# Kernel optimization log

Measured on AMD Instinct MI355X. Metric: run time of the kernel, lower is better.

Reference implementation:

```python
import jax, jax.numpy as jnp
import numpy as np
from jax import lax

N_P = 0.5      # module_cfg.n_p
CUTOFF = 0.3   # module_cfg.cutoff


def setup_inputs() -> dict:
    key = jax.random.key(0)
    k1, k2, k3, k4 = jax.random.split(key, 4)
    h = jax.random.normal(k1, (1, 8192, 256), jnp.float32)
    pos = jax.random.normal(k2, (8192, 3), jnp.float32)
    W = jax.random.normal(k3, (256, 256), jnp.float32) / 16.0  # ~ Linear init scale
    b = jax.random.normal(k4, (256,), jnp.float32) * 0.01
    return {"h": h, "pos": pos, "W": W, "b": b}


def fps_indices(pos, k, select=0):
    """Farthest point sampling; returns the k selected indices in ascending
    index order (matching torch boolean-mask indexing pos[selected])."""
    n = pos.shape[0]
    selected = jnp.zeros(n, dtype=bool).at[select].set(True)
    d = jnp.linalg.norm(pos - pos[select], axis=-1)  # (N,) euclidean, as torch.pairwise_distance
    d = jnp.where(selected, -jnp.inf, d)

    def body(i, carry):
        sel, dist = carry
        new = jnp.argmax(dist)
        sel = sel.at[new].set(True)
        dist = jnp.minimum(dist, jnp.linalg.norm(pos - pos[new], axis=-1))
        dist = jnp.where(sel, -jnp.inf, dist)
        return sel, dist

    sel, _ = lax.fori_loop(0, k - 1, body, (selected, d))
    return jnp.nonzero(sel, size=k)[0]  # exactly k True entries, sorted


def reference(h, pos, W, b):
    B, num_res, c_s = h.shape
    n_nodes = int(num_res * N_P)  # num_res * n_p // 1

    idx = fps_indices(pos, n_nodes)          # (n_nodes,)
    new_node_pos = pos[idx]                  # (n_nodes, 3)

    # torch.cdist(pos, new_node_pos, p=3): Minkowski p=3 distance
    diff = jnp.abs(pos[:, None, :] - new_node_pos[None, :, :])  # (N, n_nodes, 3)
    dist = jnp.cbrt(jnp.sum(diff ** 3, axis=-1))                 # (N, n_nodes)

    # sparse membership mask (fixed-shape equivalent of the nonzero edge list)
    mask = dist < CUTOFF                      # (N, n_nodes) bool

    # sparse gather-matmul: aggregate residue features into each sampled node
    agg = jnp.einsum('nm,bnc->bmc', mask.astype(h.dtype), h)     # (B, n_nodes, c_s)
    new_node_embed = agg @ W.T + b            # nn.Linear(c_s, c_s)
    return new_node_embed, new_node_pos, mask
```

## Files before the change

kernel.cpp:

```cpp
#include <hip/hip_runtime.h>
#include <hip/hip_bf16.h>
#include <cmath>

#define FPS_N 8192
#define FPS_K 4096
#define CS    256
#define FT    1024
#define PPT   8
#define NEGINF (-__builtin_inff())
#define FPS_LDS_BYTES (131072 + 256)

__device__ __forceinline__ float p3sum(float x, float y, float z,
                                       float nx, float ny, float nz) {
  float dx = fabsf(__fsub_rn(x, nx));
  float dy = fabsf(__fsub_rn(y, ny));
  float dz = fabsf(__fsub_rn(z, nz));
  float cx = __fmul_rn(__fmul_rn(dx, dx), dx);
  float cy = __fmul_rn(__fmul_rn(dy, dy), dy);
  float cz = __fmul_rn(__fmul_rn(dz, dz), dz);
  return __fadd_rn(__fadd_rn(cx, cy), cz);
}

__device__ __forceinline__ float eucl2(float x, float y, float z,
                                       float nx, float ny, float nz) {
  float dx = __fsub_rn(x, nx);
  float dy = __fsub_rn(y, ny);
  float dz = __fsub_rn(z, nz);
  return __fadd_rn(__fadd_rn(__fmul_rn(dx, dx), __fmul_rn(dy, dy)),
                   __fmul_rn(dz, dz));
}

#define LEXGT(va, ka, vb, kb) (((va) > (vb)) || ((va) == (vb) && ((ka) < (kb))))
#define SELP(va, ka, vb, kb) { bool t_ = LEXGT(vb, kb, va, ka); \
  va = t_ ? (vb) : (va); ka = t_ ? (kb) : (ka); }

template<int CTRL>
__device__ __forceinline__ void dpp_sel2(float& v, int& k) {
  int nv = __builtin_amdgcn_update_dpp(__float_as_int(v), __float_as_int(v), CTRL, 0xF, 0xF, false);
  int nk = __builtin_amdgcn_update_dpp(k, k, CTRL, 0xF, 0xF, false);
  float fv = __int_as_float(nv);
  bool t = LEXGT(fv, nk, v, k);
  v = t ? fv : v;
  k = t ? nk : k;
}

__global__ __launch_bounds__(1024) void bin_kernel(const float* __restrict__ pos,
                                                   float* __restrict__ px,
                                                   float* __restrict__ py,
                                                   float* __restrict__ pz,
                                                   unsigned short* __restrict__ ids16,
                                                   unsigned char* __restrict__ selb) {
  __shared__ int hist[4096];
  __shared__ int part[1024];
  const int tid = threadIdx.x;
#pragma unroll
  for (int i = 0; i < 4; ++i) hist[tid * 4 + i] = 0;
  ((int*)selb)[tid * 2 + 0] = 0;
  ((int*)selb)[tid * 2 + 1] = 0;
  if (tid == 0) selb[0] = 1;
  __syncthreads();

  float qx[8], qy[8], qz[8];
  int cell[8];
  {
    const float4* p4 = (const float4*)pos + tid * 6;
    float4 a0 = p4[0], a1 = p4[1], a2 = p4[2], a3 = p4[3], a4 = p4[4], a5 = p4[5];
    qx[0]=a0.x; qy[0]=a0.y; qz[0]=a0.z;
    qx[1]=a0.w; qy[1]=a1.x; qz[1]=a1.y;
    qx[2]=a1.z; qy[2]=a1.w; qz[2]=a2.x;
    qx[3]=a2.y; qy[3]=a2.z; qz[3]=a2.w;
    qx[4]=a3.x; qy[4]=a3.y; qz[4]=a3.z;
    qx[5]=a3.w; qy[5]=a4.x; qz[5]=a4.y;
    qx[6]=a4.z; qy[6]=a4.w; qz[6]=a5.x;
    qx[7]=a5.y; qy[7]=a5.z; qz[7]=a5.w;
  }
#pragma unroll
  for (int j = 0; j < 8; ++j) {
    int ix = min(max((int)floorf((qx[j] + 4.0f) * 2.0f), 0), 15);
    int iy = min(max((int)floorf((qy[j] + 4.0f) * 2.0f), 0), 15);
    int iz = min(max((int)floorf((qz[j] + 4.0f) * 2.0f), 0), 15);
    int m = 0;
#pragma unroll
    for (int b = 0; b < 4; ++b)
      m |= (((ix >> b) & 1) << (3 * b)) | (((iy >> b) & 1) << (3 * b + 1)) |
           (((iz >> b) & 1) << (3 * b + 2));
    cell[j] = m;
    atomicAdd(&hist[m], 1);
  }
  __syncthreads();
  int h0 = hist[tid * 4], h1 = hist[tid * 4 + 1], h2 = hist[tid * 4 + 2], h3 = hist[tid * 4 + 3];
  int s = h0 + h1 + h2 + h3;
  part[tid] = s;
  __syncthreads();
  for (int off = 1; off < 1024; off <<= 1) {
    int u = (tid >= off) ? part[tid - off] : 0;
    __syncthreads();
    part[tid] += u;
    __syncthreads();
  }
  int base = part[tid] - s;
  hist[tid * 4 + 0] = base;
  hist[tid * 4 + 1] = base + h0;
  hist[tid * 4 + 2] = base + h0 + h1;
  hist[tid * 4 + 3] = base + h0 + h1 + h2;
  __syncthreads();
#pragma unroll
  for (int j = 0; j < 8; ++j) {
    int slot = atomicAdd(&hist[cell[j]], 1);
    px[slot] = qx[j];
    py[slot] = qy[j];
    pz[slot] = qz[j];
    ids16[slot] = (unsigned short)(tid * 8 + j);
  }
}

#define RESCAN() { \
  float v0 = dd[0], v1 = dd[1], v2 = dd[2], v3 = dd[3]; \
  float v4 = dd[4], v5 = dd[5], v6 = dd[6], v7 = dd[7]; \
  int j0 = key[0], j1 = key[1], j2 = key[2], j3 = key[3]; \
  int j4 = key[4], j5 = key[5], j6 = key[6], j7 = key[7]; \
  SELP(v0, j0, v1, j1) SELP(v2, j2, v3, j3) SELP(v4, j4, v5, j5) SELP(v6, j6, v7, j7) \
  SELP(v0, j0, v2, j2) SELP(v4, j4, v6, j6) SELP(v0, j0, v4, j4) \
  bv = v0; bkey = j0; }

__global__ __launch_bounds__(FT) void fps_kernel(const float* __restrict__ pos,
                                                 const float* __restrict__ spx,
                                                 const float* __restrict__ spy,
                                                 const float* __restrict__ spz,
                                                 const unsigned short* __restrict__ sid,
                                                 unsigned char* __restrict__ selb) {
  extern __shared__ char smem[];
  float4* lds4 = (float4*)smem;
  int2*   slots = (int2*)(smem + 131072);
  const int tid = threadIdx.x, lane = tid & 63, wave = tid >> 6;

  for (int i = tid; i < FPS_N; i += FT)
    lds4[i] = make_float4(spx[i], spy[i], spz[i], 0.f);
  __syncthreads();

  float x[PPT], y[PPT], z[PPT], dd[PPT];
  int key[PPT];
  const float p0x = pos[0], p0y = pos[1], p0z = pos[2];
  {
    int4 b0 = ((const int4*)sid)[tid];
    int op[4] = { b0.x, b0.y, b0.z, b0.w };
#pragma unroll
    for (int j = 0; j < PPT; ++j) {
      int oid = (j & 1) ? ((op[j >> 1] >> 16) & 0xffff) : (op[j >> 1] & 0xffff);
      key[j] = (oid << 13) | (tid * PPT + j);
      float4 p = lds4[tid * PPT + j];
      x[j] = p.x; y[j] = p.y; z[j] = p.z;
      float s = eucl2(p.x, p.y, p.z, p0x, p0y, p0z);
      dd[j] = (oid == 0) ? NEGINF : sqrtf(s);
    }
  }
  float mnx = x[0], mny = y[0], mnz = z[0], mxx = x[0], mxy = y[0], mxz = z[0];
#pragma unroll
  for (int j = 1; j < PPT; ++j) {
    mnx = fminf(mnx, x[j]); mny = fminf(mny, y[j]); mnz = fminf(mnz, z[j]);
    mxx = fmaxf(mxx, x[j]); mxy = fmaxf(mxy, y[j]); mxz = fmaxf(mxz, z[j]);
  }

  unsigned selmask = 0;
  float bv; int bkey;
  RESCAN();
  {
    float rv = bv; int rk = bkey;
    dpp_sel2<0x111>(rv, rk); dpp_sel2<0x112>(rv, rk); dpp_sel2<0x114>(rv, rk);
    dpp_sel2<0x118>(rv, rk); dpp_sel2<0x142>(rv, rk); dpp_sel2<0x143>(rv, rk);
    if (lane == 63) slots[wave] = make_int2(__float_as_int(rv), rk);
  }
  __syncthreads();

  for (int k = 0; k < FPS_K - 1; ++k) {
    const int p = k & 1, pn = p ^ 1;
    const int2 sl = slots[p * 16 + (lane & 15)];
    float gv = __int_as_float(sl.x);
    int   gk = sl.y;
    dpp_sel2<0xB1>(gv, gk);
    dpp_sel2<0x4E>(gv, gk);
    dpp_sel2<0x124>(gv, gk);
    dpp_sel2<0x128>(gv, gk);
    const int stor = gk & 8191;

    const float4 wrec = lds4[stor];
    const float wx = wrec.x, wy = wrec.y, wz = wrec.z;

    bool own = false;
    if ((stor >> 3) == tid) {
      const int jj = stor & 7;
#pragma unroll
      for (int j = 0; j < PPT; ++j) if (j == jj) dd[j] = NEGINF;
      selmask |= (1u << jj);
      own = true;
    }

    const float lg = fmaxf(bv, 0.f);
    float cx = fminf(fmaxf(wx, mnx), mxx);
    float cy = fminf(fmaxf(wy, mny), mxy);
    float cz = fminf(fmaxf(wz, mnz), mxz);
    float ddx = wx - cx, ddy = wy - cy, ddz = wz - cz;
    float bd2 = ddx * ddx + ddy * ddy + ddz * ddz;
    const bool fire = (bd2 * 0.999f < lg * lg);
    if (fire) {
#pragma unroll
      for (int j = 0; j < PPT; ++j)
        dd[j] = fminf(dd[j], sqrtf(eucl2(x[j], y[j], z[j], wx, wy, wz)));
    }

    if (__ballot((fire || own) ? 1 : 0)) {
      if (fire || own) { RESCAN(); }
      float rv = bv; int rk = bkey;
      dpp_sel2<0x111>(rv, rk); dpp_sel2<0x112>(rv, rk); dpp_sel2<0x114>(rv, rk);
      dpp_sel2<0x118>(rv, rk); dpp_sel2<0x142>(rv, rk); dpp_sel2<0x143>(rv, rk);
      if (lane == 63) slots[pn * 16 + wave] = make_int2(__float_as_int(rv), rk);
    } else {
      if (lane == wave) slots[pn * 16 + wave] = sl;
    }
    __syncthreads();
  }

#pragma unroll
  for (int j = 0; j < PPT; ++j)
    if ((selmask >> j) & 1) selb[key[j] >> 13] = 1;
}

__global__ __launch_bounds__(1024) void emit_kernel(const unsigned char* __restrict__ selb,
                                                    const float* __restrict__ pos,
                                                    float* __restrict__ pos_out) {
  __shared__ int sc[1024];
  const int tid = threadIdx.x;
  int w0 = ((const int*)selb)[tid * 2 + 0];
  int w1 = ((const int*)selb)[tid * 2 + 1];
  int cnt = __popc(w0) + __popc(w1);
  sc[tid] = cnt;
  __syncthreads();
  for (int off = 1; off < 1024; off <<= 1) {
    int u = (tid >= off) ? sc[tid - off] : 0;
    __syncthreads();
    sc[tid] += u;
    __syncthreads();
  }
  int r = sc[tid] - cnt;
#pragma unroll
  for (int j = 0; j < 8; ++j) {
    int w = (j < 4) ? w0 : w1;
    if ((w >> ((j & 3) * 8)) & 1) {
      int oi = tid * 8 + j;
      pos_out[r * 3 + 0] = pos[oi * 3 + 0];
      pos_out[r * 3 + 1] = pos[oi * 3 + 1];
      pos_out[r * 3 + 2] = pos[oi * 3 + 2];
      ++r;
    }
  }
}

__global__ __launch_bounds__(256) void wt_kernel(const float* __restrict__ W,
                                                 float* __restrict__ WT) {
  int i = blockIdx.x * 256 + threadIdx.x;
  int c = i >> 8, cp = i & 255;
  WT[i] = W[cp * 256 + c];
}

__global__ __launch_bounds__(256) void agg_linear_kernel(
    const float* __restrict__ h, const float* __restrict__ pos,
    const float* __restrict__ nodepos, const float* __restrict__ WT,
    const float* __restrict__ bias, float* __restrict__ embed, float sb) {
  const int m = blockIdx.x;
  const int tid = threadIdx.x;
  const int lane = tid & 63, wave = tid >> 6;
  const float nx = nodepos[m * 3 + 0];
  const float ny = nodepos[m * 3 + 1];
  const float nz = nodepos[m * 3 + 2];
  const float4* h4 = (const float4*)h;

  float4 acc = make_float4(0.f, 0.f, 0.f, 0.f);
  const int base0 = wave * (FPS_N / 4);
  for (int base = base0; base < base0 + (FPS_N / 4); base += 64) {
    int n = base + lane;
    float px = pos[n * 3 + 0], py = pos[n * 3 + 1], pz = pos[n * 3 + 2];
    unsigned long long mb = __ballot((p3sum(px, py, pz, nx, ny, nz) <= sb) ? 1 : 0);
    while (mb) {
      int b = __ffsll(mb) - 1;
      mb &= (mb - 1);
      float4 hv = h4[(size_t)(base + b) * 64 + lane];
      acc.x += hv.x; acc.y += hv.y; acc.z += hv.z; acc.w += hv.w;
    }
  }

  __shared__ float lacc[4][256];
  lacc[wave][lane * 4 + 0] = acc.x;
  lacc[wave][lane * 4 + 1] = acc.y;
  lacc[wave][lane * 4 + 2] = acc.z;
  lacc[wave][lane * 4 + 3] = acc.w;
  __syncthreads();
  __shared__ float aggrow[256];
  float aggv = ((lacc[0][tid] + lacc[1][tid]) + lacc[2][tid]) + lacc[3][tid];
  aggrow[tid] = aggv;
  __syncthreads();

  float o = bias[tid];
#pragma unroll 8
  for (int c = 0; c < 256; ++c)
    o = fmaf(aggrow[c], WT[c * 256 + tid], o);
  embed[(size_t)m * 256 + tid] = o;
}

__global__ __launch_bounds__(256) void mask_kernel(const float* __restrict__ pos,
                                                   const float* __restrict__ nodepos,
                                                   float* __restrict__ maskout,
                                                   float sb) {
  int n  = blockIdx.y;
  int m0 = (blockIdx.x * 256 + threadIdx.x) * 4;
  float x = pos[n * 3 + 0], y = pos[n * 3 + 1], z = pos[n * 3 + 2];
  const float4* np4 = (const float4*)(nodepos + (size_t)m0 * 3);
  float4 a = np4[0], bq = np4[1], cq = np4[2];
  float4 r;
  r.x = (p3sum(x, y, z, a.x,  a.y,  a.z)  <= sb) ? 1.0f : 0.0f;
  r.y = (p3sum(x, y, z, a.w,  bq.x, bq.y) <= sb) ? 1.0f : 0.0f;
  r.z = (p3sum(x, y, z, bq.z, bq.w, cq.x) <= sb) ? 1.0f : 0.0f;
  r.w = (p3sum(x, y, z, cq.y, cq.z, cq.w) <= sb) ? 1.0f : 0.0f;
  *(float4*)(maskout + (size_t)n * FPS_K + m0) = r;
}

extern "C" void kernel_launch(void* const* d_in, const int* in_sizes, int n_in,
                              void* d_out, int out_size, void* d_ws, size_t ws_size,
                              hipStream_t stream) {
  (void)in_sizes; (void)n_in; (void)out_size; (void)d_ws; (void)ws_size;
  const float* h   = (const float*)d_in[0];
  const float* pos = (const float*)d_in[1];
  const float* W   = (const float*)d_in[2];
  const float* b   = (const float*)d_in[3];

  float* out     = (float*)d_out;
  float* embed   = out;
  float* pos_out = out + (size_t)FPS_K * CS;
  float* mask    = pos_out + (size_t)FPS_K * 3;
  float* WT      = mask;
  float* px      = mask + (1 << 21);
  float* py      = px + FPS_N;
  float* pz      = py + FPS_N;
  unsigned short* ids16 = (unsigned short*)(pz + FPS_N);
  unsigned char*  selb  = ((unsigned char*)ids16) + 2 * FPS_N;

  const float  t    = 0.3f;
  const float  ulpv = nextafterf(t, 1.0f) - t;
  const double rmid = (double)t - (double)ulpv * 0.5;
  const double C    = rmid * rmid * rmid;
  float sb = (float)C;
  if (!((double)sb < C)) sb = nextafterf(sb, 0.0f);

  hipFuncSetAttribute((const void*)fps_kernel,
                      hipFuncAttributeMaxDynamicSharedMemorySize, FPS_LDS_BYTES);

  hipLaunchKernelGGL(bin_kernel, dim3(1), dim3(1024), 0, stream,
                     pos, px, py, pz, ids16, selb);
  hipLaunchKernelGGL(fps_kernel, dim3(1), dim3(FT), FPS_LDS_BYTES, stream,
                     pos, px, py, pz, ids16, selb);
  hipLaunchKernelGGL(emit_kernel, dim3(1), dim3(1024), 0, stream,
                     selb, pos, pos_out);
  hipLaunchKernelGGL(wt_kernel, dim3(256), dim3(256), 0, stream, W, WT);
  hipLaunchKernelGGL(agg_linear_kernel, dim3(FPS_K), dim3(256), 0, stream,
                     h, pos, pos_out, WT, b, embed, sb);
  hipLaunchKernelGGL(mask_kernel, dim3(4, FPS_N), dim3(256), 0, stream,
                     pos, pos_out, mask, sb);
}
```

Measured before the change: 6.913 ms.

## Select up to four FPS points per barrier using per-wave top-2 candidates

The FPS loop now keeps the top two candidates per wave, together with their coordinates, in shared slots. Each iteration can then accept up to four successive farthest points without a block-wide barrier. A candidate is accepted only when its distance to the points already accepted in that batch is at least its own value, so the greedy order is preserved. This also drops the 128KB LDS copy of point coordinates, because coordinates now travel with the slot records. The aim is to cut the number of __syncthreads rounds in the serial 4095-step loop, at the cost of more DPP traffic per step and more complex reduction logic.

```diff
diff --git a/kernel.cpp b/kernel.cpp
--- a/kernel.cpp
+++ b/kernel.cpp
@@ -8,7 +8,6 @@
 #define FT    1024
 #define PPT   8
 #define NEGINF (-__builtin_inff())
-#define FPS_LDS_BYTES (131072 + 256)
 
 __device__ __forceinline__ float p3sum(float x, float y, float z,
                                        float nx, float ny, float nz) {
@@ -31,18 +30,91 @@
 }
 
 #define LEXGT(va, ka, vb, kb) (((va) > (vb)) || ((va) == (vb) && ((ka) < (kb))))
-#define SELP(va, ka, vb, kb) { bool t_ = LEXGT(vb, kb, va, ka); \
-  va = t_ ? (vb) : (va); ka = t_ ? (kb) : (ka); }
 
 template<int CTRL>
-__device__ __forceinline__ void dpp_sel2(float& v, int& k) {
-  int nv = __builtin_amdgcn_update_dpp(__float_as_int(v), __float_as_int(v), CTRL, 0xF, 0xF, false);
-  int nk = __builtin_amdgcn_update_dpp(k, k, CTRL, 0xF, 0xF, false);
-  float fv = __int_as_float(nv);
-  bool t = LEXGT(fv, nk, v, k);
-  v = t ? fv : v;
-  k = t ? nk : k;
-}
+__device__ __forceinline__ int dppi(int a) {
+  return __builtin_amdgcn_update_dpp(a, a, CTRL, 0xF, 0xF, false);
+}
+template<int CTRL>
+__device__ __forceinline__ float dppf(float a) {
+  return __int_as_float(__builtin_amdgcn_update_dpp(__float_as_int(a), __float_as_int(a), CTRL, 0xF, 0xF, false));
+}
+
+template<int CTRL>
+__device__ __forceinline__ void dpp_sel5(float& v, int& k, float& x, float& y, float& z) {
+  float pv = dppf<CTRL>(v); int pk = dppi<CTRL>(k);
+  float px = dppf<CTRL>(x); float py = dppf<CTRL>(y); float pz = dppf<CTRL>(z);
+  bool t = LEXGT(pv, pk, v, k);
+  v = t ? pv : v; k = t ? pk : k;
+  x = t ? px : x; y = t ? py : y; z = t ? pz : z;
+}
+
+template<int CTRL>
+__device__ __forceinline__ void dpp_top2(float& v1, int& k1, float& v2, int& k2) {
+  float p1 = dppf<CTRL>(v1); int q1 = dppi<CTRL>(k1);
+  float p2 = dppf<CTRL>(v2); int q2 = dppi<CTRL>(k2);
+  bool t = LEXGT(p1, q1, v1, k1);
+  float lv = t ? v1 : p1; int lk = t ? k1 : q1;
+  float ov = t ? p2 : v2; int ok = t ? q2 : k2;
+  v1 = t ? p1 : v1; k1 = t ? q1 : k1;
+  bool u = LEXGT(lv, lk, ov, ok);
+  v2 = u ? lv : ov; k2 = u ? lk : ok;
+}
+
+#define PAIR2(v1, k1, v2, k2, a, ka, b, kb) { bool t_ = LEXGT(b, kb, a, ka); \
+  v1 = t_ ? (b) : (a); k1 = t_ ? (kb) : (ka); v2 = t_ ? (a) : (b); k2 = t_ ? (ka) : (kb); }
+
+#define MERGE22(v1, k1, v2, k2, w1, l1, w2, l2) { \
+  bool t_ = LEXGT(w1, l1, v1, k1); \
+  float lv_ = t_ ? (v1) : (w1); int lk_ = t_ ? (k1) : (l1); \
+  float ov_ = t_ ? (w2) : (v2); int ok_ = t_ ? (l2) : (k2); \
+  v1 = t_ ? (w1) : (v1); k1 = t_ ? (l1) : (k1); \
+  bool u_ = LEXGT(lv_, lk_, ov_, ok_); \
+  v2 = u_ ? lv_ : ov_; k2 = u_ ? lk_ : ok_; }
+
+#define RESCAN2() { \
+  float A1, B1, C1, D1, A2, B2, C2, D2; int Ak, Bk, Ck, Dk, Ak2, Bk2, Ck2, Dk2; \
+  PAIR2(A1, Ak, A2, Ak2, dd[0], key[0], dd[1], key[1]) \
+  PAIR2(B1, Bk, B2, Bk2, dd[2], key[2], dd[3], key[3]) \
+  PAIR2(C1, Ck, C2, Ck2, dd[4], key[4], dd[5], key[5]) \
+  PAIR2(D1, Dk, D2, Dk2, dd[6], key[6], dd[7], key[7]) \
+  MERGE22(A1, Ak, A2, Ak2, B1, Bk, B2, Bk2) \
+  MERGE22(C1, Ck, C2, Ck2, D1, Dk, D2, Dk2) \
+  MERGE22(A1, Ak, A2, Ak2, C1, Ck, C2, Ck2) \
+  bv = A1; bkey = Ak; bv2 = A2; bk2 = Ak2; }
+
+#define WAVE_PUBLISH2(sn) { \
+  float rv1 = bv; int rk1 = bkey; float rv2 = bv2; int rk2 = bk2; \
+  dpp_top2<0x111>(rv1, rk1, rv2, rk2); dpp_top2<0x112>(rv1, rk1, rv2, rk2); \
+  dpp_top2<0x114>(rv1, rk1, rv2, rk2); dpp_top2<0x118>(rv1, rk1, rv2, rk2); \
+  dpp_top2<0x142>(rv1, rk1, rv2, rk2); dpp_top2<0x143>(rv1, rk1, rv2, rk2); \
+  const int k1u = __builtin_amdgcn_readlane(rk1, 63); \
+  const int v2u = __builtin_amdgcn_readlane(__float_as_int(rv2), 63); \
+  const int k2u = __builtin_amdgcn_readlane(rk2, 63); \
+  int* s_ = &slots[(sn) * 192 + wave * 12]; \
+  if (bkey == k1u) { \
+    float sx = x[0], sy = y[0], sz = z[0]; \
+    _Pragma("unroll") \
+    for (int j = 0; j < PPT; ++j) \
+      if (j == (bkey & 7)) { sx = x[j]; sy = y[j]; sz = z[j]; } \
+    s_[0] = __float_as_int(bv); s_[1] = bkey; \
+    s_[2] = __float_as_int(sx); s_[3] = __float_as_int(sy); s_[4] = __float_as_int(sz); \
+    if (bk2 == k2u) { \
+      float tx = x[0], ty = y[0], tz = z[0]; \
+      _Pragma("unroll") \
+      for (int j = 0; j < PPT; ++j) \
+        if (j == (bk2 & 7)) { tx = x[j]; ty = y[j]; tz = z[j]; } \
+      s_[5] = v2u; s_[6] = k2u; \
+      s_[7] = __float_as_int(tx); s_[8] = __float_as_int(ty); s_[9] = __float_as_int(tz); \
+    } \
+  } else if (bkey == k2u) { \
+    float sx = x[0], sy = y[0], sz = z[0]; \
+    _Pragma("unroll") \
+    for (int j = 0; j < PPT; ++j) \
+      if (j == (bkey & 7)) { sx = x[j]; sy = y[j]; sz = z[j]; } \
+    s_[5] = __float_as_int(bv); s_[6] = bkey; \
+    s_[7] = __float_as_int(sx); s_[8] = __float_as_int(sy); s_[9] = __float_as_int(sz); \
+  } }
 
 __global__ __launch_bounds__(1024) void bin_kernel(const float* __restrict__ pos,
                                                    float* __restrict__ px,
@@ -88,7 +160,7 @@
     atomicAdd(&hist[m], 1);
   }
   __syncthreads();
-  int h0 = hist[tid * 4], h1 = hist[tid * 4 + 1], h2 = hist[tid * 4 + 2], h3 = hist[tid * 4 + 3];
+  int h0 = hist[tid*4], h1 = hist[tid*4+1], h2 = hist[tid*4+2], h3 = hist[tid*4+3];
   int s = h0 + h1 + h2 + h3;
   part[tid] = s;
   __syncthreads();
@@ -99,10 +171,10 @@
     __syncthreads();
   }
   int base = part[tid] - s;
-  hist[tid * 4 + 0] = base;
-  hist[tid * 4 + 1] = base + h0;
-  hist[tid * 4 + 2] = base + h0 + h1;
-  hist[tid * 4 + 3] = base + h0 + h1 + h2;
+  hist[tid*4+0] = base;
+  hist[tid*4+1] = base + h0;
+  hist[tid*4+2] = base + h0 + h1;
+  hist[tid*4+3] = base + h0 + h1 + h2;
   __syncthreads();
 #pragma unroll
   for (int j = 0; j < 8; ++j) {
@@ -114,29 +186,14 @@
   }
 }
 
-#define RESCAN() { \
-  float v0 = dd[0], v1 = dd[1], v2 = dd[2], v3 = dd[3]; \
-  float v4 = dd[4], v5 = dd[5], v6 = dd[6], v7 = dd[7]; \
-  int j0 = key[0], j1 = key[1], j2 = key[2], j3 = key[3]; \
-  int j4 = key[4], j5 = key[5], j6 = key[6], j7 = key[7]; \
-  SELP(v0, j0, v1, j1) SELP(v2, j2, v3, j3) SELP(v4, j4, v5, j5) SELP(v6, j6, v7, j7) \
-  SELP(v0, j0, v2, j2) SELP(v4, j4, v6, j6) SELP(v0, j0, v4, j4) \
-  bv = v0; bkey = j0; }
-
 __global__ __launch_bounds__(FT) void fps_kernel(const float* __restrict__ pos,
                                                  const float* __restrict__ spx,
                                                  const float* __restrict__ spy,
                                                  const float* __restrict__ spz,
                                                  const unsigned short* __restrict__ sid,
                                                  unsigned char* __restrict__ selb) {
-  extern __shared__ char smem[];
-  float4* lds4 = (float4*)smem;
-  int2*   slots = (int2*)(smem + 131072);
+  __shared__ int slots[2 * 192];
   const int tid = threadIdx.x, lane = tid & 63, wave = tid >> 6;
-
-  for (int i = tid; i < FPS_N; i += FT)
-    lds4[i] = make_float4(spx[i], spy[i], spz[i], 0.f);
-  __syncthreads();
 
   float x[PPT], y[PPT], z[PPT], dd[PPT];
   int key[PPT];
@@ -148,9 +205,9 @@
     for (int j = 0; j < PPT; ++j) {
       int oid = (j & 1) ? ((op[j >> 1] >> 16) & 0xffff) : (op[j >> 1] & 0xffff);
       key[j] = (oid << 13) | (tid * PPT + j);
-      float4 p = lds4[tid * PPT + j];
-      x[j] = p.x; y[j] = p.y; z[j] = p.z;
-      float s = eucl2(p.x, p.y, p.z, p0x, p0y, p0z);
+      float X = spx[tid * PPT + j], Y = spy[tid * PPT + j], Z = spz[tid * PPT + j];
+      x[j] = X; y[j] = Y; z[j] = Z;
+      float s = eucl2(X, Y, Z, p0x, p0y, p0z);
       dd[j] = (oid == 0) ? NEGINF : sqrtf(s);
     }
   }
@@ -162,61 +219,101 @@
   }
 
   unsigned selmask = 0;
-  float bv; int bkey;
-  RESCAN();
-  {
-    float rv = bv; int rk = bkey;
-    dpp_sel2<0x111>(rv, rk); dpp_sel2<0x112>(rv, rk); dpp_sel2<0x114>(rv, rk);
-    dpp_sel2<0x118>(rv, rk); dpp_sel2<0x142>(rv, rk); dpp_sel2<0x143>(rv, rk);
-    if (lane == 63) slots[wave] = make_int2(__float_as_int(rv), rk);
-  }
-  __syncthreads();
-
-  for (int k = 0; k < FPS_K - 1; ++k) {
-    const int p = k & 1, pn = p ^ 1;
-    const int2 sl = slots[p * 16 + (lane & 15)];
-    float gv = __int_as_float(sl.x);
-    int   gk = sl.y;
-    dpp_sel2<0xB1>(gv, gk);
-    dpp_sel2<0x4E>(gv, gk);
-    dpp_sel2<0x124>(gv, gk);
-    dpp_sel2<0x128>(gv, gk);
-    const int stor = gk & 8191;
-
-    const float4 wrec = lds4[stor];
-    const float wx = wrec.x, wy = wrec.y, wz = wrec.z;
-
-    bool own = false;
-    if ((stor >> 3) == tid) {
-      const int jj = stor & 7;
-#pragma unroll
-      for (int j = 0; j < PPT; ++j) if (j == jj) dd[j] = NEGINF;
-      selmask |= (1u << jj);
-      own = true;
-    }
+  float bv, bv2; int bkey, bk2;
+  RESCAN2();
+  WAVE_PUBLISH2(0);
+  __syncthreads();
+
+  int sel = 0, p = 0;
+  while (sel < FPS_K - 1) {
+    const int pn = p ^ 1;
+    const int row = lane & 15;
+    const int4 q0 = *(const int4*)&slots[p * 192 + row * 12 + 0];
+    const int4 q1 = *(const int4*)&slots[p * 192 + row * 12 + 4];
+    const int4 q2 = *(const int4*)&slots[p * 192 + row * 12 + 8];
+    float ev = __int_as_float(q0.x); int ek = q0.y;
+    float ex = __int_as_float(q0.z), ey = __int_as_float(q0.w), ez = __int_as_float(q1.x);
+    const float sv2 = __int_as_float(q1.y); const int sk2 = q1.z;
+    const float sx2 = __int_as_float(q1.w), sy2 = __int_as_float(q2.x), sz2 = __int_as_float(q2.y);
+    bool avail2 = true;
+
+    int A = 0;
+    bool stop = false, own = false, fire = false;
+    const int cap = FPS_K - 1 - sel;
+    float a0x=0, a0y=0, a0z=0, a1x=0, a1y=0, a1z=0, a2x=0, a2y=0, a2z=0, a3x=0, a3y=0, a3z=0;
+
+#define PSTEP(AX, AY, AZ, ACCCHK) \
+    if (!stop) { \
+      float mv = ev; int mk = ek; float mx = ex, my = ey, mz = ez; \
+      dpp_sel5<0xB1>(mv, mk, mx, my, mz); \
+      dpp_sel5<0x4E>(mv, mk, mx, my, mz); \
+      dpp_sel5<0x124>(mv, mk, mx, my, mz); \
+      dpp_sel5<0x128>(mv, mk, mx, my, mz); \
+      bool ok = true; \
+      ACCCHK \
+      if (!ok) stop = true; \
+      else { \
+        AX = mx; AY = my; AZ = mz; \
+        const int stor = mk & 8191; \
+        if ((stor >> 3) == tid) { \
+          const int jj = stor & 7; \
+          _Pragma("unroll") \
+          for (int j = 0; j < PPT; ++j) if (j == jj) dd[j] = NEGINF; \
+          selmask |= (1u << jj); \
+          own = true; \
+        } \
+        const int ww = stor >> 9; \
+        if (row == ww) { \
+          if (avail2) { ev = sv2; ek = sk2; ex = sx2; ey = sy2; ez = sz2; avail2 = false; } \
+          else { ev = NEGINF; ek = 0x7fffffff; } \
+        } \
+        ++A; \
+        if (A >= cap || A >= 4) stop = true; \
+      } \
+    }
+
+    PSTEP(a0x, a0y, a0z, )
+    PSTEP(a1x, a1y, a1z,
+      ok = (sqrtf(eucl2(mx, my, mz, a0x, a0y, a0z)) >= mv);)
+    PSTEP(a2x, a2y, a2z,
+      ok = (sqrtf(eucl2(mx, my, mz, a0x, a0y, a0z)) >= mv)
+        && (sqrtf(eucl2(mx, my, mz, a1x, a1y, a1z)) >= mv);)
+    PSTEP(a3x, a3y, a3z,
+      ok = (sqrtf(eucl2(mx, my, mz, a0x, a0y, a0z)) >= mv)
+        && (sqrtf(eucl2(mx, my, mz, a1x, a1y, a1z)) >= mv)
+        && (sqrtf(eucl2(mx, my, mz, a2x, a2y, a2z)) >= mv);)
+#undef PSTEP
 
     const float lg = fmaxf(bv, 0.f);
-    float cx = fminf(fmaxf(wx, mnx), mxx);
-    float cy = fminf(fmaxf(wy, mny), mxy);
-    float cz = fminf(fmaxf(wz, mnz), mxz);
-    float ddx = wx - cx, ddy = wy - cy, ddz = wz - cz;
-    float bd2 = ddx * ddx + ddy * ddy + ddz * ddz;
-    const bool fire = (bd2 * 0.999f < lg * lg);
-    if (fire) {
-#pragma unroll
-      for (int j = 0; j < PPT; ++j)
-        dd[j] = fminf(dd[j], sqrtf(eucl2(x[j], y[j], z[j], wx, wy, wz)));
-    }
+    const float lg2 = lg * lg;
+#define UPDC(c, AX, AY, AZ) \
+    if ((c) < A) { \
+      float cx = fminf(fmaxf(AX, mnx), mxx); \
+      float cy = fminf(fmaxf(AY, mny), mxy); \
+      float cz = fminf(fmaxf(AZ, mnz), mxz); \
+      float ddx = AX - cx, ddy = AY - cy, ddz = AZ - cz; \
+      float bd2 = ddx * ddx + ddy * ddy + ddz * ddz; \
+      if (bd2 * 0.999f < lg2) { \
+        _Pragma("unroll") \
+        for (int j = 0; j < PPT; ++j) \
+          dd[j] = fminf(dd[j], sqrtf(eucl2(x[j], y[j], z[j], AX, AY, AZ))); \
+        fire = true; \
+      } \
+    }
+    UPDC(0, a0x, a0y, a0z)
+    UPDC(1, a1x, a1y, a1z)
+    UPDC(2, a2x, a2y, a2z)
+    UPDC(3, a3x, a3y, a3z)
+#undef UPDC
 
     if (__ballot((fire || own) ? 1 : 0)) {
-      if (fire || own) { RESCAN(); }
-      float rv = bv; int rk = bkey;
-      dpp_sel2<0x111>(rv, rk); dpp_sel2<0x112>(rv, rk); dpp_sel2<0x114>(rv, rk);
-      dpp_sel2<0x118>(rv, rk); dpp_sel2<0x142>(rv, rk); dpp_sel2<0x143>(rv, rk);
-      if (lane == 63) slots[pn * 16 + wave] = make_int2(__float_as_int(rv), rk);
+      if (fire || own) { RESCAN2(); }
+      WAVE_PUBLISH2(pn);
     } else {
-      if (lane == wave) slots[pn * 16 + wave] = sl;
-    }
+      if (lane < 12) slots[pn * 192 + wave * 12 + lane] = slots[p * 192 + wave * 12 + lane];
+    }
+    sel += A;
+    p = pn;
     __syncthreads();
   }
 
@@ -278,8 +375,8 @@
   const int base0 = wave * (FPS_N / 4);
   for (int base = base0; base < base0 + (FPS_N / 4); base += 64) {
     int n = base + lane;
-    float px = pos[n * 3 + 0], py = pos[n * 3 + 1], pz = pos[n * 3 + 2];
-    unsigned long long mb = __ballot((p3sum(px, py, pz, nx, ny, nz) <= sb) ? 1 : 0);
+    float qx = pos[n * 3 + 0], qy = pos[n * 3 + 1], qz = pos[n * 3 + 2];
+    unsigned long long mb = __ballot((p3sum(qx, qy, qz, nx, ny, nz) <= sb) ? 1 : 0);
     while (mb) {
       int b = __ffsll(mb) - 1;
       mb &= (mb - 1);
@@ -350,12 +447,9 @@
   float sb = (float)C;
   if (!((double)sb < C)) sb = nextafterf(sb, 0.0f);
 
-  hipFuncSetAttribute((const void*)fps_kernel,
-                      hipFuncAttributeMaxDynamicSharedMemorySize, FPS_LDS_BYTES);
-
   hipLaunchKernelGGL(bin_kernel, dim3(1), dim3(1024), 0, stream,
                      pos, px, py, pz, ids16, selb);
-  hipLaunchKernelGGL(fps_kernel, dim3(1), dim3(FT), FPS_LDS_BYTES, stream,
+  hipLaunchKernelGGL(fps_kernel, dim3(1), dim3(FT), 0, stream,
                      pos, px, py, pz, ids16, selb);
   hipLaunchKernelGGL(emit_kernel, dim3(1), dim3(1024), 0, stream,
                      selb, pos, pos_out);
```

New measurement: 7.297 ms. +5.6%, slower.

## Rewrite FPS as single-wave lazy per-group updates with top-2 caching

Applied to the files above, without the earlier changes.

Farthest point sampling now runs in one 64-lane wave instead of a 1024-thread block, which removes the per-iteration __syncthreads. Each lane owns a spatial group of 128 points held in LDS and caches its top-2 candidates. Distance updates for newly selected points are deferred into a per-group pending list and applied only when that group's candidate is chosen while stale. Cross-wave barriers are traded for serialized per-group recomputation inside a single wave, which could cost more when many groups are dirty.

```diff
diff --git a/kernel.cpp b/kernel.cpp
--- a/kernel.cpp
+++ b/kernel.cpp
@@ -5,10 +5,9 @@
 #define FPS_N 8192
 #define FPS_K 4096
 #define CS    256
-#define FT    1024
-#define PPT   8
 #define NEGINF (-__builtin_inff())
-#define FPS_LDS_BYTES (131072 + 256)
+#define KMAX  0x7fffffff
+#define FPS_LDS 155648
 
 __device__ __forceinline__ float p3sum(float x, float y, float z,
                                        float nx, float ny, float nz) {
@@ -31,18 +30,40 @@
 }
 
 #define LEXGT(va, ka, vb, kb) (((va) > (vb)) || ((va) == (vb) && ((ka) < (kb))))
-#define SELP(va, ka, vb, kb) { bool t_ = LEXGT(vb, kb, va, ka); \
-  va = t_ ? (vb) : (va); ka = t_ ? (kb) : (ka); }
+#define GMASK(i) ((i) ^ (((i) >> 7) & 31))
+
+template<int CTRL>
+__device__ __forceinline__ int dppi(int a) {
+  return __builtin_amdgcn_update_dpp(a, a, CTRL, 0xF, 0xF, false);
+}
+template<int CTRL>
+__device__ __forceinline__ float dppf(float a) {
+  return __int_as_float(__builtin_amdgcn_update_dpp(__float_as_int(a), __float_as_int(a), CTRL, 0xF, 0xF, false));
+}
 
 template<int CTRL>
 __device__ __forceinline__ void dpp_sel2(float& v, int& k) {
-  int nv = __builtin_amdgcn_update_dpp(__float_as_int(v), __float_as_int(v), CTRL, 0xF, 0xF, false);
-  int nk = __builtin_amdgcn_update_dpp(k, k, CTRL, 0xF, 0xF, false);
-  float fv = __int_as_float(nv);
+  float fv = dppf<CTRL>(v);
+  int   nk = dppi<CTRL>(k);
   bool t = LEXGT(fv, nk, v, k);
   v = t ? fv : v;
   k = t ? nk : k;
 }
+
+template<int CTRL>
+__device__ __forceinline__ void dpp_top2(float& v1, int& k1, float& v2, int& k2) {
+  float p1 = dppf<CTRL>(v1); int q1 = dppi<CTRL>(k1);
+  float p2 = dppf<CTRL>(v2); int q2 = dppi<CTRL>(k2);
+  bool t = LEXGT(p1, q1, v1, k1);
+  float lv = t ? v1 : p1; int lk = t ? k1 : q1;
+  float ov = t ? p2 : v2; int ok = t ? q2 : k2;
+  v1 = t ? p1 : v1; k1 = t ? q1 : k1;
+  bool u = LEXGT(lv, lk, ov, ok);
+  v2 = u ? lv : ov; k2 = u ? lk : ok;
+}
+
+#define PAIR2(v1, k1, v2, k2, a, ka, b, kb) { bool t_ = LEXGT(b, kb, a, ka); \
+  v1 = t_ ? (b) : (a); k1 = t_ ? (kb) : (ka); v2 = t_ ? (a) : (b); k2 = t_ ? (ka) : (kb); }
 
 __global__ __launch_bounds__(1024) void bin_kernel(const float* __restrict__ pos,
                                                    float* __restrict__ px,
@@ -88,7 +109,7 @@
     atomicAdd(&hist[m], 1);
   }
   __syncthreads();
-  int h0 = hist[tid * 4], h1 = hist[tid * 4 + 1], h2 = hist[tid * 4 + 2], h3 = hist[tid * 4 + 3];
+  int h0 = hist[tid*4], h1 = hist[tid*4+1], h2 = hist[tid*4+2], h3 = hist[tid*4+3];
   int s = h0 + h1 + h2 + h3;
   part[tid] = s;
   __syncthreads();
@@ -99,10 +120,10 @@
     __syncthreads();
   }
   int base = part[tid] - s;
-  hist[tid * 4 + 0] = base;
-  hist[tid * 4 + 1] = base + h0;
-  hist[tid * 4 + 2] = base + h0 + h1;
-  hist[tid * 4 + 3] = base + h0 + h1 + h2;
+  hist[tid*4+0] = base;
+  hist[tid*4+1] = base + h0;
+  hist[tid*4+2] = base + h0 + h1;
+  hist[tid*4+3] = base + h0 + h1 + h2;
   __syncthreads();
 #pragma unroll
   for (int j = 0; j < 8; ++j) {
@@ -114,115 +135,135 @@
   }
 }
 
-#define RESCAN() { \
-  float v0 = dd[0], v1 = dd[1], v2 = dd[2], v3 = dd[3]; \
-  float v4 = dd[4], v5 = dd[5], v6 = dd[6], v7 = dd[7]; \
-  int j0 = key[0], j1 = key[1], j2 = key[2], j3 = key[3]; \
-  int j4 = key[4], j5 = key[5], j6 = key[6], j7 = key[7]; \
-  SELP(v0, j0, v1, j1) SELP(v2, j2, v3, j3) SELP(v4, j4, v5, j5) SELP(v6, j6, v7, j7) \
-  SELP(v0, j0, v2, j2) SELP(v4, j4, v6, j6) SELP(v0, j0, v4, j4) \
-  bv = v0; bkey = j0; }
-
-__global__ __launch_bounds__(FT) void fps_kernel(const float* __restrict__ pos,
+__global__ __launch_bounds__(64) void fps_kernel(const float* __restrict__ pos,
                                                  const float* __restrict__ spx,
                                                  const float* __restrict__ spy,
                                                  const float* __restrict__ spz,
                                                  const unsigned short* __restrict__ sid,
                                                  unsigned char* __restrict__ selb) {
   extern __shared__ char smem[];
-  float4* lds4 = (float4*)smem;
-  int2*   slots = (int2*)(smem + 131072);
-  const int tid = threadIdx.x, lane = tid & 63, wave = tid >> 6;
-
-  for (int i = tid; i < FPS_N; i += FT)
-    lds4[i] = make_float4(spx[i], spy[i], spz[i], 0.f);
-  __syncthreads();
-
-  float x[PPT], y[PPT], z[PPT], dd[PPT];
-  int key[PPT];
+  float* ddL = (float*)smem;
+  float* xL  = (float*)(smem + 32768);
+  float* yL  = (float*)(smem + 65536);
+  float* zL  = (float*)(smem + 98304);
+  unsigned short* pend  = (unsigned short*)(smem + 131072);
+  unsigned short* clogi = (unsigned short*)(smem + 147456);
+  const int lane = threadIdx.x;
+
   const float p0x = pos[0], p0y = pos[1], p0z = pos[2];
+  for (int i = lane; i < FPS_N; i += 64) {
+    float X = spx[i], Y = spy[i], Z = spz[i];
+    int oid = sid[i];
+    float s = eucl2(X, Y, Z, p0x, p0y, p0z);
+    float dv = (oid == 0) ? NEGINF : sqrtf(s);
+    int ph = GMASK(i);
+    xL[ph] = X; yL[ph] = Y; zL[ph] = Z; ddL[ph] = dv;
+  }
+
+  float gb = NEGINF, g2v = NEGINF;
+  int   gkey = KMAX, g2k = KMAX;
+  float bnx = 1e30f, bny = 1e30f, bnz = 1e30f;
+  float bxx = -1e30f, bxy = -1e30f, bxz = -1e30f;
   {
-    int4 b0 = ((const int4*)sid)[tid];
-    int op[4] = { b0.x, b0.y, b0.z, b0.w };
-#pragma unroll
-    for (int j = 0; j < PPT; ++j) {
-      int oid = (j & 1) ? ((op[j >> 1] >> 16) & 0xffff) : (op[j >> 1] & 0xffff);
-      key[j] = (oid << 13) | (tid * PPT + j);
-      float4 p = lds4[tid * PPT + j];
-      x[j] = p.x; y[j] = p.y; z[j] = p.z;
-      float s = eucl2(p.x, p.y, p.z, p0x, p0y, p0z);
-      dd[j] = (oid == 0) ? NEGINF : sqrtf(s);
-    }
-  }
-  float mnx = x[0], mny = y[0], mnz = z[0], mxx = x[0], mxy = y[0], mxz = z[0];
-#pragma unroll
-  for (int j = 1; j < PPT; ++j) {
-    mnx = fminf(mnx, x[j]); mny = fminf(mny, y[j]); mnz = fminf(mnz, z[j]);
-    mxx = fmaxf(mxx, x[j]); mxy = fmaxf(mxy, y[j]); mxz = fmaxf(mxz, z[j]);
-  }
-
-  unsigned selmask = 0;
-  float bv; int bkey;
-  RESCAN();
-  {
-    float rv = bv; int rk = bkey;
-    dpp_sel2<0x111>(rv, rk); dpp_sel2<0x112>(rv, rk); dpp_sel2<0x114>(rv, rk);
-    dpp_sel2<0x118>(rv, rk); dpp_sel2<0x142>(rv, rk); dpp_sel2<0x143>(rv, rk);
-    if (lane == 63) slots[wave] = make_int2(__float_as_int(rv), rk);
-  }
-  __syncthreads();
-
-  for (int k = 0; k < FPS_K - 1; ++k) {
-    const int p = k & 1, pn = p ^ 1;
-    const int2 sl = slots[p * 16 + (lane & 15)];
-    float gv = __int_as_float(sl.x);
-    int   gk = sl.y;
-    dpp_sel2<0xB1>(gv, gk);
-    dpp_sel2<0x4E>(gv, gk);
-    dpp_sel2<0x124>(gv, gk);
-    dpp_sel2<0x128>(gv, gk);
-    const int stor = gk & 8191;
-
-    const float4 wrec = lds4[stor];
-    const float wx = wrec.x, wy = wrec.y, wz = wrec.z;
-
-    bool own = false;
-    if ((stor >> 3) == tid) {
-      const int jj = stor & 7;
-#pragma unroll
-      for (int j = 0; j < PPT; ++j) if (j == jj) dd[j] = NEGINF;
-      selmask |= (1u << jj);
-      own = true;
-    }
-
-    const float lg = fmaxf(bv, 0.f);
-    float cx = fminf(fmaxf(wx, mnx), mxx);
-    float cy = fminf(fmaxf(wy, mny), mxy);
-    float cz = fminf(fmaxf(wz, mnz), mxz);
+    const int base = lane << 7;
+    for (int t = 0; t < 128; ++t) {
+      int i = base + t, ph = GMASK(i);
+      float X = xL[ph], Y = yL[ph], Z = zL[ph], dv = ddL[ph];
+      bnx = fminf(bnx, X); bny = fminf(bny, Y); bnz = fminf(bnz, Z);
+      bxx = fmaxf(bxx, X); bxy = fmaxf(bxy, Y); bxz = fmaxf(bxz, Z);
+      int kk = ((int)sid[i] << 13) | i;
+      bool b1 = LEXGT(dv, kk, gb, gkey);
+      bool b2 = LEXGT(dv, kk, g2v, g2k);
+      float ov = gb; int ok = gkey;
+      gb  = b1 ? dv : gb;   gkey = b1 ? kk : gkey;
+      g2v = b1 ? ov : (b2 ? dv : g2v);
+      g2k = b1 ? ok : (b2 ? kk : g2k);
+    }
+  }
+
+  bool dirty = false, avail2 = true, ovf = false;
+  int pcount = 0, lastref = 0;
+  int sel = 0;
+
+  while (sel < FPS_K - 1) {
+    float tv = gb; int tk = gkey;
+    dpp_sel2<0x111>(tv, tk); dpp_sel2<0x112>(tv, tk); dpp_sel2<0x114>(tv, tk);
+    dpp_sel2<0x118>(tv, tk); dpp_sel2<0x142>(tv, tk); dpp_sel2<0x143>(tv, tk);
+    const int wk = __builtin_amdgcn_readlane(tk, 63);
+    const int stor = wk & 8191;
+    const int g = stor >> 7;
+    const unsigned long long dmask = __ballot(dirty ? 1 : 0);
+
+    if ((dmask >> g) & 1) {
+      const int i0 = (g << 7) + lane, i1 = i0 + 64;
+      const int ph0 = GMASK(i0), ph1 = GMASK(i1);
+      float d0 = ddL[ph0], d1 = ddL[ph1];
+      const float X0 = xL[ph0], Y0 = yL[ph0], Z0 = zL[ph0];
+      const float X1 = xL[ph1], Y1 = yL[ph1], Z1 = zL[ph1];
+      const int oid0 = sid[i0], oid1 = sid[i1];
+      const unsigned long long omask = __ballot(ovf ? 1 : 0);
+      if (!((omask >> g) & 1)) {
+        const int P = __builtin_amdgcn_readlane(pcount, g);
+        for (int t = 0; t < P; ++t) {
+          int cp = GMASK((int)pend[(g << 7) + t]);
+          float ax = xL[cp], ay = yL[cp], az = zL[cp];
+          d0 = fminf(d0, sqrtf(eucl2(X0, Y0, Z0, ax, ay, az)));
+          d1 = fminf(d1, sqrtf(eucl2(X1, Y1, Z1, ax, ay, az)));
+        }
+      } else {
+        const int L0 = __builtin_amdgcn_readlane(lastref, g);
+        for (int t = L0; t < sel; ++t) {
+          int cp = GMASK((int)clogi[t]);
+          float ax = xL[cp], ay = yL[cp], az = zL[cp];
+          d0 = fminf(d0, sqrtf(eucl2(X0, Y0, Z0, ax, ay, az)));
+          d1 = fminf(d1, sqrtf(eucl2(X1, Y1, Z1, ax, ay, az)));
+        }
+      }
+      ddL[ph0] = d0; ddL[ph1] = d1;
+      int k0 = (oid0 << 13) | i0, k1 = (oid1 << 13) | i1;
+      float v1, v2; int kk1, kk2;
+      PAIR2(v1, kk1, v2, kk2, d0, k0, d1, k1)
+      dpp_top2<0x111>(v1, kk1, v2, kk2); dpp_top2<0x112>(v1, kk1, v2, kk2);
+      dpp_top2<0x114>(v1, kk1, v2, kk2); dpp_top2<0x118>(v1, kk1, v2, kk2);
+      dpp_top2<0x142>(v1, kk1, v2, kk2); dpp_top2<0x143>(v1, kk1, v2, kk2);
+      const int nv1 = __builtin_amdgcn_readlane(__float_as_int(v1), 63);
+      const int nk1 = __builtin_amdgcn_readlane(kk1, 63);
+      const int nv2 = __builtin_amdgcn_readlane(__float_as_int(v2), 63);
+      const int nk2 = __builtin_amdgcn_readlane(kk2, 63);
+      if (lane == g) {
+        gb  = __int_as_float(nv1); gkey = nk1;
+        g2v = __int_as_float(nv2); g2k  = nk2;
+        avail2 = true; dirty = false; ovf = false; pcount = 0; lastref = sel;
+      }
+      continue;
+    }
+
+    const int ph = GMASK(stor);
+    const float wx = xL[ph], wy = yL[ph], wz = zL[ph];
+    if (lane == 0) {
+      ddL[ph] = NEGINF;
+      selb[wk >> 13] = 1;
+      clogi[sel] = (unsigned short)stor;
+    }
+    if (lane == g) {
+      if (avail2) { gb = g2v; gkey = g2k; avail2 = false; }
+      else dirty = true;
+    }
+    float lg = fmaxf(gb, 0.f);
+    float cx = fminf(fmaxf(wx, bnx), bxx);
+    float cy = fminf(fmaxf(wy, bny), bxy);
+    float cz = fminf(fmaxf(wz, bnz), bxz);
     float ddx = wx - cx, ddy = wy - cy, ddz = wz - cz;
     float bd2 = ddx * ddx + ddy * ddy + ddz * ddz;
-    const bool fire = (bd2 * 0.999f < lg * lg);
-    if (fire) {
-#pragma unroll
-      for (int j = 0; j < PPT; ++j)
-        dd[j] = fminf(dd[j], sqrtf(eucl2(x[j], y[j], z[j], wx, wy, wz)));
-    }
-
-    if (__ballot((fire || own) ? 1 : 0)) {
-      if (fire || own) { RESCAN(); }
-      float rv = bv; int rk = bkey;
-      dpp_sel2<0x111>(rv, rk); dpp_sel2<0x112>(rv, rk); dpp_sel2<0x114>(rv, rk);
-      dpp_sel2<0x118>(rv, rk); dpp_sel2<0x142>(rv, rk); dpp_sel2<0x143>(rv, rk);
-      if (lane == 63) slots[pn * 16 + wave] = make_int2(__float_as_int(rv), rk);
-    } else {
-      if (lane == wave) slots[pn * 16 + wave] = sl;
-    }
-    __syncthreads();
-  }
-
-#pragma unroll
-  for (int j = 0; j < PPT; ++j)
-    if ((selmask >> j) & 1) selb[key[j] >> 13] = 1;
+    if (bd2 * 0.999f < lg * lg) {
+      if (!ovf) {
+        if (pcount < 128) { pend[(lane << 7) + pcount] = (unsigned short)stor; ++pcount; }
+        else ovf = true;
+      }
+      dirty = true;
+    }
+    ++sel;
+  }
 }
 
 __global__ __launch_bounds__(1024) void emit_kernel(const unsigned char* __restrict__ selb,
@@ -278,8 +319,8 @@
   const int base0 = wave * (FPS_N / 4);
   for (int base = base0; base < base0 + (FPS_N / 4); base += 64) {
     int n = base + lane;
-    float px = pos[n * 3 + 0], py = pos[n * 3 + 1], pz = pos[n * 3 + 2];
-    unsigned long long mb = __ballot((p3sum(px, py, pz, nx, ny, nz) <= sb) ? 1 : 0);
+    float qx = pos[n * 3 + 0], qy = pos[n * 3 + 1], qz = pos[n * 3 + 2];
+    unsigned long long mb = __ballot((p3sum(qx, qy, qz, nx, ny, nz) <= sb) ? 1 : 0);
     while (mb) {
       int b = __ffsll(mb) - 1;
       mb &= (mb - 1);
@@ -351,11 +392,11 @@
   if (!((double)sb < C)) sb = nextafterf(sb, 0.0f);
 
   hipFuncSetAttribute((const void*)fps_kernel,
-                      hipFuncAttributeMaxDynamicSharedMemorySize, FPS_LDS_BYTES);
+                      hipFuncAttributeMaxDynamicSharedMemorySize, FPS_LDS);
 
   hipLaunchKernelGGL(bin_kernel, dim3(1), dim3(1024), 0, stream,
                      pos, px, py, pz, ids16, selb);
-  hipLaunchKernelGGL(fps_kernel, dim3(1), dim3(FT), FPS_LDS_BYTES, stream,
+  hipLaunchKernelGGL(fps_kernel, dim3(1), dim3(64), FPS_LDS, stream,
                      pos, px, py, pz, ids16, selb);
   hipLaunchKernelGGL(emit_kernel, dim3(1), dim3(1024), 0, stream,
                      selb, pos, pos_out);
```

Result: slower. 13.74 ms (+98.7%).

## Replace FPS per-iteration barrier with flag-based wave sync and carry winner coords

Applied to the files above, without the earlier changes.

The FPS loop drops the block-wide __syncthreads and uses per-wave progress counters in LDS that each wave spins on, with a triple-buffered slot array for wave winners. Each wave's winner now publishes its coordinates along with its value and key, and the DPP reduction carries them. This removes the 128KB LDS point table and the dependent LDS lookup of the chosen point. It risks spin-wait overhead and subtle memory-ordering bugs, and relies on a bounded guard counter to exit the spin.

```diff
diff --git a/kernel.cpp b/kernel.cpp
--- a/kernel.cpp
+++ b/kernel.cpp
@@ -8,7 +8,7 @@
 #define FT    1024
 #define PPT   8
 #define NEGINF (-__builtin_inff())
-#define FPS_LDS_BYTES (131072 + 256)
+#define KMAX  0x7fffffff
 
 __device__ __forceinline__ float p3sum(float x, float y, float z,
                                        float nx, float ny, float nz) {
@@ -35,14 +35,40 @@
   va = t_ ? (vb) : (va); ka = t_ ? (kb) : (ka); }
 
 template<int CTRL>
+__device__ __forceinline__ int dppi(int a) {
+  return __builtin_amdgcn_update_dpp(a, a, CTRL, 0xF, 0xF, false);
+}
+template<int CTRL>
+__device__ __forceinline__ float dppf(float a) {
+  return __int_as_float(__builtin_amdgcn_update_dpp(__float_as_int(a), __float_as_int(a), CTRL, 0xF, 0xF, false));
+}
+
+template<int CTRL>
 __device__ __forceinline__ void dpp_sel2(float& v, int& k) {
-  int nv = __builtin_amdgcn_update_dpp(__float_as_int(v), __float_as_int(v), CTRL, 0xF, 0xF, false);
-  int nk = __builtin_amdgcn_update_dpp(k, k, CTRL, 0xF, 0xF, false);
-  float fv = __int_as_float(nv);
+  float fv = dppf<CTRL>(v);
+  int   nk = dppi<CTRL>(k);
   bool t = LEXGT(fv, nk, v, k);
   v = t ? fv : v;
   k = t ? nk : k;
 }
+
+template<int CTRL>
+__device__ __forceinline__ void dpp_sel5(float& v, int& k, float& x, float& y, float& z) {
+  float pv = dppf<CTRL>(v); int pk = dppi<CTRL>(k);
+  float px = dppf<CTRL>(x); float py = dppf<CTRL>(y); float pz = dppf<CTRL>(z);
+  bool t = LEXGT(pv, pk, v, k);
+  v = t ? pv : v; k = t ? pk : k;
+  x = t ? px : x; y = t ? py : y; z = t ? pz : z;
+}
+
+#define RESCAN() { \
+  float v0 = dd[0], v1 = dd[1], v2 = dd[2], v3 = dd[3]; \
+  float v4 = dd[4], v5 = dd[5], v6 = dd[6], v7 = dd[7]; \
+  int j0 = key[0], j1 = key[1], j2 = key[2], j3 = key[3]; \
+  int j4 = key[4], j5 = key[5], j6 = key[6], j7 = key[7]; \
+  SELP(v0, j0, v1, j1) SELP(v2, j2, v3, j3) SELP(v4, j4, v5, j5) SELP(v6, j6, v7, j7) \
+  SELP(v0, j0, v2, j2) SELP(v4, j4, v6, j6) SELP(v0, j0, v4, j4) \
+  bv = v0; bkey = j0; }
 
 __global__ __launch_bounds__(1024) void bin_kernel(const float* __restrict__ pos,
                                                    float* __restrict__ px,
@@ -88,7 +114,7 @@
     atomicAdd(&hist[m], 1);
   }
   __syncthreads();
-  int h0 = hist[tid * 4], h1 = hist[tid * 4 + 1], h2 = hist[tid * 4 + 2], h3 = hist[tid * 4 + 3];
+  int h0 = hist[tid*4], h1 = hist[tid*4+1], h2 = hist[tid*4+2], h3 = hist[tid*4+3];
   int s = h0 + h1 + h2 + h3;
   part[tid] = s;
   __syncthreads();
@@ -99,10 +125,10 @@
     __syncthreads();
   }
   int base = part[tid] - s;
-  hist[tid * 4 + 0] = base;
-  hist[tid * 4 + 1] = base + h0;
-  hist[tid * 4 + 2] = base + h0 + h1;
-  hist[tid * 4 + 3] = base + h0 + h1 + h2;
+  hist[tid*4+0] = base;
+  hist[tid*4+1] = base + h0;
+  hist[tid*4+2] = base + h0 + h1;
+  hist[tid*4+3] = base + h0 + h1 + h2;
   __syncthreads();
 #pragma unroll
   for (int j = 0; j < 8; ++j) {
@@ -114,29 +140,16 @@
   }
 }
 
-#define RESCAN() { \
-  float v0 = dd[0], v1 = dd[1], v2 = dd[2], v3 = dd[3]; \
-  float v4 = dd[4], v5 = dd[5], v6 = dd[6], v7 = dd[7]; \
-  int j0 = key[0], j1 = key[1], j2 = key[2], j3 = key[3]; \
-  int j4 = key[4], j5 = key[5], j6 = key[6], j7 = key[7]; \
-  SELP(v0, j0, v1, j1) SELP(v2, j2, v3, j3) SELP(v4, j4, v5, j5) SELP(v6, j6, v7, j7) \
-  SELP(v0, j0, v2, j2) SELP(v4, j4, v6, j6) SELP(v0, j0, v4, j4) \
-  bv = v0; bkey = j0; }
-
 __global__ __launch_bounds__(FT) void fps_kernel(const float* __restrict__ pos,
                                                  const float* __restrict__ spx,
                                                  const float* __restrict__ spy,
                                                  const float* __restrict__ spz,
                                                  const unsigned short* __restrict__ sid,
                                                  unsigned char* __restrict__ selb) {
-  extern __shared__ char smem[];
-  float4* lds4 = (float4*)smem;
-  int2*   slots = (int2*)(smem + 131072);
+  __shared__ __align__(16) int sS[3][16][12];
+  __shared__ int sT[16];
+  volatile int* vT = sT;
   const int tid = threadIdx.x, lane = tid & 63, wave = tid >> 6;
-
-  for (int i = tid; i < FPS_N; i += FT)
-    lds4[i] = make_float4(spx[i], spy[i], spz[i], 0.f);
-  __syncthreads();
 
   float x[PPT], y[PPT], z[PPT], dd[PPT];
   int key[PPT];
@@ -148,9 +161,9 @@
     for (int j = 0; j < PPT; ++j) {
       int oid = (j & 1) ? ((op[j >> 1] >> 16) & 0xffff) : (op[j >> 1] & 0xffff);
       key[j] = (oid << 13) | (tid * PPT + j);
-      float4 p = lds4[tid * PPT + j];
-      x[j] = p.x; y[j] = p.y; z[j] = p.z;
-      float s = eucl2(p.x, p.y, p.z, p0x, p0y, p0z);
+      float X = spx[tid * PPT + j], Y = spy[tid * PPT + j], Z = spz[tid * PPT + j];
+      x[j] = X; y[j] = Y; z[j] = Z;
+      float s = eucl2(X, Y, Z, p0x, p0y, p0z);
       dd[j] = (oid == 0) ? NEGINF : sqrtf(s);
     }
   }
@@ -168,23 +181,47 @@
     float rv = bv; int rk = bkey;
     dpp_sel2<0x111>(rv, rk); dpp_sel2<0x112>(rv, rk); dpp_sel2<0x114>(rv, rk);
     dpp_sel2<0x118>(rv, rk); dpp_sel2<0x142>(rv, rk); dpp_sel2<0x143>(rv, rk);
-    if (lane == 63) slots[wave] = make_int2(__float_as_int(rv), rk);
+    int wkk = __builtin_amdgcn_readlane(rk, 63);
+    if (bkey == wkk) {
+      float sx = x[0], sy = y[0], sz = z[0];
+#pragma unroll
+      for (int j = 0; j < PPT; ++j)
+        if (j == (bkey & 7)) { sx = x[j]; sy = y[j]; sz = z[j]; }
+      *(int4*)&sS[0][wave][0] = make_int4(__float_as_int(bv), bkey,
+                                          __float_as_int(sx), __float_as_int(sy));
+      sS[0][wave][4] = __float_as_int(sz);
+    }
+    if (lane == wave) sT[wave] = 0;
   }
   __syncthreads();
 
   for (int k = 0; k < FPS_K - 1; ++k) {
-    const int p = k & 1, pn = p ^ 1;
-    const int2 sl = slots[p * 16 + (lane & 15)];
-    float gv = __int_as_float(sl.x);
-    int   gk = sl.y;
-    dpp_sel2<0xB1>(gv, gk);
-    dpp_sel2<0x4E>(gv, gk);
-    dpp_sel2<0x124>(gv, gk);
-    dpp_sel2<0x128>(gv, gk);
+    const int pk = k % 3, pw = (k + 1) % 3;
+    if (k > 0) {
+      int guard = 0;
+      while (true) {
+        int t = vT[lane & 15];
+        if (__ballot(t < k) == 0ULL) break;
+        if (++guard > (1 << 22)) break;
+      }
+      __builtin_amdgcn_sched_barrier(0);
+      __asm__ volatile("" ::: "memory");
+    }
+
+    const int* rowp = &sS[pk][lane & 15][0];
+    const int4 q0 = *(const int4*)rowp;
+    const int  qz4 = rowp[4];
+    float gv = __int_as_float(q0.x);
+    int   gk = q0.y;
+    float gx = __int_as_float(q0.z);
+    float gy = __int_as_float(q0.w);
+    float gz = __int_as_float(qz4);
+
+    dpp_sel5<0xB1>(gv, gk, gx, gy, gz);
+    dpp_sel5<0x4E>(gv, gk, gx, gy, gz);
+    dpp_sel5<0x124>(gv, gk, gx, gy, gz);
+    dpp_sel5<0x128>(gv, gk, gx, gy, gz);
     const int stor = gk & 8191;
-
-    const float4 wrec = lds4[stor];
-    const float wx = wrec.x, wy = wrec.y, wz = wrec.z;
 
     bool own = false;
     if ((stor >> 3) == tid) {
@@ -196,16 +233,16 @@
     }
 
     const float lg = fmaxf(bv, 0.f);
-    float cx = fminf(fmaxf(wx, mnx), mxx);
-    float cy = fminf(fmaxf(wy, mny), mxy);
-    float cz = fminf(fmaxf(wz, mnz), mxz);
-    float ddx = wx - cx, ddy = wy - cy, ddz = wz - cz;
+    float cx = fminf(fmaxf(gx, mnx), mxx);
+    float cy = fminf(fmaxf(gy, mny), mxy);
+    float cz = fminf(fmaxf(gz, mnz), mxz);
+    float ddx = gx - cx, ddy = gy - cy, ddz = gz - cz;
     float bd2 = ddx * ddx + ddy * ddy + ddz * ddz;
     const bool fire = (bd2 * 0.999f < lg * lg);
     if (fire) {
 #pragma unroll
       for (int j = 0; j < PPT; ++j)
-        dd[j] = fminf(dd[j], sqrtf(eucl2(x[j], y[j], z[j], wx, wy, wz)));
+        dd[j] = fminf(dd[j], sqrtf(eucl2(x[j], y[j], z[j], gx, gy, gz)));
     }
 
     if (__ballot((fire || own) ? 1 : 0)) {
@@ -213,11 +250,24 @@
       float rv = bv; int rk = bkey;
       dpp_sel2<0x111>(rv, rk); dpp_sel2<0x112>(rv, rk); dpp_sel2<0x114>(rv, rk);
       dpp_sel2<0x118>(rv, rk); dpp_sel2<0x142>(rv, rk); dpp_sel2<0x143>(rv, rk);
-      if (lane == 63) slots[pn * 16 + wave] = make_int2(__float_as_int(rv), rk);
+      int wkk = __builtin_amdgcn_readlane(rk, 63);
+      if (bkey == wkk) {
+        float sx = x[0], sy = y[0], sz = z[0];
+#pragma unroll
+        for (int j = 0; j < PPT; ++j)
+          if (j == (bkey & 7)) { sx = x[j]; sy = y[j]; sz = z[j]; }
+        *(int4*)&sS[pw][wave][0] = make_int4(__float_as_int(bv), bkey,
+                                             __float_as_int(sx), __float_as_int(sy));
+        sS[pw][wave][4] = __float_as_int(sz);
+      }
     } else {
-      if (lane == wave) slots[pn * 16 + wave] = sl;
-    }
-    __syncthreads();
+      if (lane == wave) {
+        *(int4*)&sS[pw][wave][0] = q0;
+        sS[pw][wave][4] = qz4;
+      }
+    }
+    __asm__ volatile("s_waitcnt lgkmcnt(0)" ::: "memory");
+    if (lane == wave) vT[wave] = k + 1;
   }
 
 #pragma unroll
@@ -278,8 +328,8 @@
   const int base0 = wave * (FPS_N / 4);
   for (int base = base0; base < base0 + (FPS_N / 4); base += 64) {
     int n = base + lane;
-    float px = pos[n * 3 + 0], py = pos[n * 3 + 1], pz = pos[n * 3 + 2];
-    unsigned long long mb = __ballot((p3sum(px, py, pz, nx, ny, nz) <= sb) ? 1 : 0);
+    float qx = pos[n * 3 + 0], qy = pos[n * 3 + 1], qz = pos[n * 3 + 2];
+    unsigned long long mb = __ballot((p3sum(qx, qy, qz, nx, ny, nz) <= sb) ? 1 : 0);
     while (mb) {
       int b = __ffsll(mb) - 1;
       mb &= (mb - 1);
@@ -350,12 +400,9 @@
   float sb = (float)C;
   if (!((double)sb < C)) sb = nextafterf(sb, 0.0f);
 
-  hipFuncSetAttribute((const void*)fps_kernel,
-                      hipFuncAttributeMaxDynamicSharedMemorySize, FPS_LDS_BYTES);
-
   hipLaunchKernelGGL(bin_kernel, dim3(1), dim3(1024), 0, stream,
                      pos, px, py, pz, ids16, selb);
-  hipLaunchKernelGGL(fps_kernel, dim3(1), dim3(FT), FPS_LDS_BYTES, stream,
+  hipLaunchKernelGGL(fps_kernel, dim3(1), dim3(FT), 0, stream,
                      pos, px, py, pz, ids16, selb);
   hipLaunchKernelGGL(emit_kernel, dim3(1), dim3(1024), 0, stream,
                      selb, pos, pos_out);
```

Result: slower. 9.789 ms (+41.6%).
